# Kernel optimization log

Hardware: AMD Instinct MI355X
Metric: run time of the kernel (lower is better)

Reference implementation:

```python
import jax, jax.numpy as jnp
import numpy as np

N = 1_000_000   # total nodes
F = 128         # num_node_features
P = 16          # num_graph_coordinators
G = 128         # graphs in batch


def setup_inputs() -> dict:
    key = jax.random.key(0)
    k_x, k_p, k_b = jax.random.split(key, 3)
    learnable_param = jax.random.normal(k_p, (P, F), dtype=jnp.float32)
    # last_updated_param is a deepcopy of learnable_param at init time
    last_updated_param = learnable_param
    x = jax.random.normal(k_x, (N, F), dtype=jnp.float32)
    # seed exact copies of coordinator params into x so matches occur
    # (mirrors add_learnable_features_with_no_grad appending coordinator rows)
    seed_idx = jnp.arange(P) * (N // P)  # P well-separated rows
    x = x.at[seed_idx].set(last_updated_param)
    batch = jnp.sort(jax.random.randint(k_b, (N,), 0, G)).astype(jnp.int64)
    return {"x": x, "batch": batch,
            "learnable_param": learnable_param,
            "last_updated_param": last_updated_param}


def reference(x, batch, learnable_param, last_updated_param):
    # For every node row, check exact equality against each last_updated_param
    # the enumerate loop where each match overwrites the row). Comparisons run
    # against the running (already-replaced) x, matching the in-place torch
    # semantics. batch/graph grouping does not affect the result: every node is
    # visited exactly once regardless of loop order.
    def body(x_cur, pair):
        last_p, learn_p = pair  # [F], [F]
        m = jnp.all(x_cur == last_p[None, :], axis=1)  # [N] exact row match
        x_new = jnp.where(m[:, None], learn_p[None, :], x_cur)
        return x_new, None

    x_out, _ = jax.lax.scan(body, x, (last_updated_param, learnable_param))
    return x_out
```

## Files before the change

kernel.cpp:

```cpp
#include <hip/hip_runtime.h>


#define F_DIM 128
#define P_DIM 16
#define CAND_CAP 8192
#define UNROLL 4

typedef float f32x4 __attribute__((ext_vector_type(4)));

__global__ void init_counter_kernel(int* ws) {
    if (threadIdx.x == 0 && blockIdx.x == 0) ws[0] = 0;
}

__global__ __launch_bounds__(256) void copy_scan_kernel(
    const float* __restrict__ x,
    const float* __restrict__ last,
    float* __restrict__ out,
    int* __restrict__ ws,
    int n_rows)
{
    float sig[P_DIM];
    #pragma unroll
    for (int p = 0; p < P_DIM; ++p) sig[p] = last[p * F_DIM];

    const f32x4* __restrict__ src = reinterpret_cast<const f32x4*>(x);
    f32x4*       __restrict__ dst = reinterpret_cast<f32x4*>(out);

    const int tid     = threadIdx.x;
    const int total4  = n_rows * (F_DIM / 4);
    const int chunk   = blockDim.x * UNROLL;
    const int gstride = chunk * gridDim.x;

    for (int base = blockIdx.x * chunk; base < total4; base += gstride) {
        const int i0 = base + tid;

        f32x4 v[UNROLL];
        #pragma unroll
        for (int m = 0; m < UNROLL; ++m) {
            const int i4 = i0 + m * 256;
            if (i4 < total4)
                v[m] = __builtin_nontemporal_load(&src[i4]);
        }

        if ((tid & 31) == 0) {
            #pragma unroll
            for (int m = 0; m < UNROLL; ++m) {
                const int i4 = i0 + m * 256;
                if (i4 < total4) {
                    bool any = false;
                    #pragma unroll
                    for (int p = 0; p < P_DIM; ++p) any |= (v[m].x == sig[p]);
                    if (any) {
                        const int slot = atomicAdd(ws, 1);
                        if (slot < CAND_CAP) ws[1 + slot] = i4 >> 5;
                    }
                }
            }
        }

        #pragma unroll
        for (int m = 0; m < UNROLL; ++m) {
            const int i4 = i0 + m * 256;
            if (i4 < total4)
                __builtin_nontemporal_store(v[m], &dst[i4]);
        }
    }
}

__global__ __launch_bounds__(256) void fixup_kernel(
    const float* __restrict__ x,
    const float* __restrict__ learn,
    const float* __restrict__ last,
    float* __restrict__ out,
    const int* __restrict__ ws)
{
    const int n_cand = min(ws[0], CAND_CAP);
    const int lane = threadIdx.x & 63;
    const int wave = threadIdx.x >> 6;
    const int n_waves = blockDim.x >> 6;

    for (int c = wave; c < n_cand; c += n_waves) {
        const int row = ws[1 + c];
        float v0 = x[(size_t)row * F_DIM + lane];
        float v1 = x[(size_t)row * F_DIM + 64 + lane];

        for (int p = 0; p < P_DIM; ++p) {
            const float l0 = last[p * F_DIM + lane];
            const float l1 = last[p * F_DIM + 64 + lane];
            const bool eq = (v0 == l0) & (v1 == l1);
            if (__ballot(eq) == ~0ULL) {
                v0 = learn[p * F_DIM + lane];
                v1 = learn[p * F_DIM + 64 + lane];
            }
        }
        out[(size_t)row * F_DIM + lane]      = v0;
        out[(size_t)row * F_DIM + 64 + lane] = v1;
    }
}

extern "C" void kernel_launch(void* const* d_in, const int* in_sizes, int n_in,
                              void* d_out, int out_size, void* d_ws, size_t ws_size,
                              hipStream_t stream) {
    const float* x     = (const float*)d_in[0];
    const float* learn = (const float*)d_in[2];
    const float* last  = (const float*)d_in[3];
    float*       out   = (float*)d_out;
    int*         ws    = (int*)d_ws;

    const int n_rows = in_sizes[0] / F_DIM;

    init_counter_kernel<<<1, 64, 0, stream>>>(ws);
    copy_scan_kernel<<<2048, 256, 0, stream>>>(x, last, out, ws, n_rows);
    fixup_kernel<<<1, 256, 0, stream>>>(x, learn, last, out, ws);
}
```

Before: 187.4 us.

## Fuse candidate detection and row fixup into a single copy kernel

Replaces the three-kernel pipeline (counter init, copy-and-scan with an atomic candidate list, single-block fixup) with one kernel that checks matches inline and writes the corrected row directly. Wavefront-level ballot over each 32-lane half checks the full row against each parameter only when the first-element filter fires. This removes two kernel launches, the global atomic, and the serial single-block fixup that re-read candidate rows. It also splits the loop into a bounds-check-free main body and a guarded tail. The cost is a wave-wide __any and divergent branch per unrolled vector in the hot loop.

```diff
diff --git a/kernel.cpp b/kernel.cpp
--- a/kernel.cpp
+++ b/kernel.cpp
@@ -3,20 +3,15 @@
 
 #define F_DIM 128
 #define P_DIM 16
-#define CAND_CAP 8192
 #define UNROLL 4
 
 typedef float f32x4 __attribute__((ext_vector_type(4)));
 
-__global__ void init_counter_kernel(int* ws) {
-    if (threadIdx.x == 0 && blockIdx.x == 0) ws[0] = 0;
-}
-
-__global__ __launch_bounds__(256) void copy_scan_kernel(
+__global__ __launch_bounds__(256) void copy_fix_kernel(
     const float* __restrict__ x,
+    const float* __restrict__ learn,
     const float* __restrict__ last,
     float* __restrict__ out,
-    int* __restrict__ ws,
     int n_rows)
 {
     float sig[P_DIM];
@@ -26,75 +21,78 @@
     const f32x4* __restrict__ src = reinterpret_cast<const f32x4*>(x);
     f32x4*       __restrict__ dst = reinterpret_cast<f32x4*>(out);
 
-    const int tid     = threadIdx.x;
+    const int tid  = threadIdx.x;
+    const int half = (tid >> 5) & 1;
+    const int sl   = tid & 31;
+
     const int total4  = n_rows * (F_DIM / 4);
-    const int chunk   = blockDim.x * UNROLL;
+    const int chunk   = 256 * UNROLL;
     const int gstride = chunk * gridDim.x;
+    const int total4_full = total4 & ~(chunk - 1);
 
-    for (int base = blockIdx.x * chunk; base < total4; base += gstride) {
+    int base = blockIdx.x * chunk;
+    for (; base < total4_full; base += gstride) {
         const int i0 = base + tid;
 
         f32x4 v[UNROLL];
         #pragma unroll
+        for (int m = 0; m < UNROLL; ++m)
+            v[m] = __builtin_nontemporal_load(&src[i0 + m * 256]);
+
+        #pragma unroll
         for (int m = 0; m < UNROLL; ++m) {
-            const int i4 = i0 + m * 256;
-            if (i4 < total4)
-                v[m] = __builtin_nontemporal_load(&src[i4]);
-        }
-
-        if ((tid & 31) == 0) {
-            #pragma unroll
-            for (int m = 0; m < UNROLL; ++m) {
-                const int i4 = i0 + m * 256;
-                if (i4 < total4) {
-                    bool any = false;
-                    #pragma unroll
-                    for (int p = 0; p < P_DIM; ++p) any |= (v[m].x == sig[p]);
-                    if (any) {
-                        const int slot = atomicAdd(ws, 1);
-                        if (slot < CAND_CAP) ws[1 + slot] = i4 >> 5;
-                    }
+            bool hit = false;
+            if (sl == 0) {
+                #pragma unroll
+                for (int p = 0; p < P_DIM; ++p) hit |= (v[m].x == sig[p]);
+            }
+            if (__any(hit)) {
+                for (int p = 0; p < P_DIM; ++p) {
+                    const f32x4 lp =
+                        *reinterpret_cast<const f32x4*>(&last[p * F_DIM + sl * 4]);
+                    const bool eq = (v[m].x == lp.x) & (v[m].y == lp.y) &
+                                    (v[m].z == lp.z) & (v[m].w == lp.w);
+                    const unsigned long long bm = __ballot(eq);
+                    const unsigned int mh = (unsigned int)(bm >> (half * 32));
+                    if (mh == 0xFFFFFFFFu)
+                        v[m] = *reinterpret_cast<const f32x4*>(
+                                   &learn[p * F_DIM + sl * 4]);
                 }
             }
         }
 
         #pragma unroll
+        for (int m = 0; m < UNROLL; ++m)
+            __builtin_nontemporal_store(v[m], &dst[i0 + m * 256]);
+    }
+
+    for (; base < total4; base += gstride) {
+        const int i0 = base + tid;
+        #pragma unroll
         for (int m = 0; m < UNROLL; ++m) {
             const int i4 = i0 + m * 256;
-            if (i4 < total4)
-                __builtin_nontemporal_store(v[m], &dst[i4]);
+            if (i4 >= total4) continue;
+            f32x4 v = __builtin_nontemporal_load(&src[i4]);
+            bool hit = false;
+            if (sl == 0) {
+                #pragma unroll
+                for (int p = 0; p < P_DIM; ++p) hit |= (v.x == sig[p]);
+            }
+            if (__any(hit)) {
+                for (int p = 0; p < P_DIM; ++p) {
+                    const f32x4 lp =
+                        *reinterpret_cast<const f32x4*>(&last[p * F_DIM + sl * 4]);
+                    const bool eq = (v.x == lp.x) & (v.y == lp.y) &
+                                    (v.z == lp.z) & (v.w == lp.w);
+                    const unsigned long long bm = __ballot(eq);
+                    const unsigned int mh = (unsigned int)(bm >> (half * 32));
+                    if (mh == 0xFFFFFFFFu)
+                        v = *reinterpret_cast<const f32x4*>(
+                                &learn[p * F_DIM + sl * 4]);
+                }
+            }
+            __builtin_nontemporal_store(v, &dst[i4]);
         }
-    }
-}
-
-__global__ __launch_bounds__(256) void fixup_kernel(
-    const float* __restrict__ x,
-    const float* __restrict__ learn,
-    const float* __restrict__ last,
-    float* __restrict__ out,
-    const int* __restrict__ ws)
-{
-    const int n_cand = min(ws[0], CAND_CAP);
-    const int lane = threadIdx.x & 63;
-    const int wave = threadIdx.x >> 6;
-    const int n_waves = blockDim.x >> 6;
-
-    for (int c = wave; c < n_cand; c += n_waves) {
-        const int row = ws[1 + c];
-        float v0 = x[(size_t)row * F_DIM + lane];
-        float v1 = x[(size_t)row * F_DIM + 64 + lane];
-
-        for (int p = 0; p < P_DIM; ++p) {
-            const float l0 = last[p * F_DIM + lane];
-            const float l1 = last[p * F_DIM + 64 + lane];
-            const bool eq = (v0 == l0) & (v1 == l1);
-            if (__ballot(eq) == ~0ULL) {
-                v0 = learn[p * F_DIM + lane];
-                v1 = learn[p * F_DIM + 64 + lane];
-            }
-        }
-        out[(size_t)row * F_DIM + lane]      = v0;
-        out[(size_t)row * F_DIM + 64 + lane] = v1;
     }
 }
 
@@ -105,11 +103,8 @@
     const float* learn = (const float*)d_in[2];
     const float* last  = (const float*)d_in[3];
     float*       out   = (float*)d_out;
-    int*         ws    = (int*)d_ws;
 
     const int n_rows = in_sizes[0] / F_DIM;
 
-    init_counter_kernel<<<1, 64, 0, stream>>>(ws);
-    copy_scan_kernel<<<2048, 256, 0, stream>>>(x, last, out, ws, n_rows);
-    fixup_kernel<<<1, 256, 0, stream>>>(x, learn, last, out, ws);
+    copy_fix_kernel<<<2048, 256, 0, stream>>>(x, learn, last, out, n_rows);
 }
```

Result: faster. 182.4 us (-2.7%).
